# Kernel tuning notes

Measured on AMD Instinct MI355X. Metric: run time of the kernel, lower is better.

The kernel has to match this reference:

```python
import jax, jax.numpy as jnp
import numpy as np

N = 50000      # n_nodes
E = 800000     # n_edges (avg degree 16)
IN, HID, CLS = 128, 128, 40


def setup_inputs() -> dict:
    key = jax.random.key(0)
    ks = jax.random.split(key, 9)
    features = jax.random.normal(ks[0], (N, IN), dtype=jnp.float32)
    src = jax.random.randint(ks[1], (E,), 0, N)
    dst = jax.random.randint(ks[2], (E,), 0, N)
    # GraphConv weights (glorot-ish scale) and biases
    W0 = jax.random.normal(ks[3], (IN, HID), dtype=jnp.float32) / np.sqrt(IN).astype(np.float32)
    b0 = jnp.zeros((HID,), jnp.float32)
    W1 = jax.random.normal(ks[4], (HID, HID), dtype=jnp.float32) / np.sqrt(HID).astype(np.float32)
    b1 = jnp.zeros((HID,), jnp.float32)
    W2 = jax.random.normal(ks[5], (HID, CLS), dtype=jnp.float32) / np.sqrt(HID).astype(np.float32)
    b2 = jnp.zeros((CLS,), jnp.float32)
    return {"features": features, "src": src, "dst": dst,
            "W0": W0, "b0": b0, "W1": W1, "b1": b1, "W2": W2, "b2": b2}


def _degree_norms(src, dst, dtype):
    # DGL GraphConv norm='both': D_out^{-1/2} on source side, D_in^{-1/2} on dest side,
    # degrees clamped to a minimum of 1.
    ones = jnp.ones(src.shape[0], dtype)
    deg_out = jax.ops.segment_sum(ones, src, num_segments=N)
    deg_in = jax.ops.segment_sum(ones, dst, num_segments=N)
    norm_out = jnp.where(deg_out > 0, deg_out, 1.0) ** -0.5
    norm_in = jnp.where(deg_in > 0, deg_in, 1.0) ** -0.5
    return norm_out, norm_in


def _graph_conv(h, src, dst, norm_out, norm_in, W, b, act):
    # h' = D_in^{-1/2} A D_out^{-1/2} h W + b ; optional relu
    h = (h * norm_out[:, None]) @ W            # dense transform first (in >= out)
    agg = jax.ops.segment_sum(h[src], dst, num_segments=N)  # sparse aggregation
    out = agg * norm_in[:, None] + b
    return jax.nn.relu(out) if act else out


def reference(features, src, dst, W0, b0, W1, b1, W2, b2):
    norm_out, norm_in = _degree_norms(src, dst, features.dtype)
    # dropout is identity in eval mode
    h = _graph_conv(features, src, dst, norm_out, norm_in, W0, b0, True)
    h = _graph_conv(h, src, dst, norm_out, norm_in, W1, b1, True)
    h = _graph_conv(h, src, dst, norm_out, norm_in, W2, b2, False)
    return h
```

## Files before the change

kernel.cpp:

```cpp
#include <hip/hip_runtime.h>
#include <hip/hip_fp16.h>


static constexpr int NN  = 50000;
static constexpr int NE  = 800000;
static constexpr int HID = 128;
static constexpr int CLS = 40;
static constexpr int CAP = 48;

static constexpr int NGEMM  = (NN + 127) / 128;
static constexpr int NBUILD = (NE + 255) / 256;
static constexpr int NPREP  = 8;

typedef __attribute__((ext_vector_type(8))) _Float16 f16x8;
typedef __attribute__((ext_vector_type(4))) float    f32x4;

__device__ __forceinline__ void gemm128_body(const float* __restrict__ X,
                                             const float* __restrict__ W,
                                             __half* __restrict__ Y,
                                             int tileIdx, float* As, float* Bs) {
    constexpr int BSTR = 132;
    const int tid = threadIdx.x;
    const int rowBase = tileIdx * 128;

    const int bkk = tid >> 3;
    const int bc4 = tid & 7;
    const float* wrow = W + (size_t)bkk * 128 + bc4 * 16;

    const int rt = tid & 15;
    const int ct = tid >> 4;

    float acc[8][8];
    #pragma unroll
    for (int j = 0; j < 8; ++j)
        #pragma unroll
        for (int i = 0; i < 8; ++i) acc[j][i] = 0.f;

    float4 xv[4], wv[4];

    auto loadA = [&](int s) {
        #pragma unroll
        for (int i = 0; i < 4; ++i) {
            int f = tid + 256 * i;
            int r = f >> 3;
            int kc = f & 7;
            int grow = rowBase + r;
            xv[i] = (grow < NN)
                ? *(const float4*)(X + (size_t)grow * 128 + s * 32 + kc * 4)
                : make_float4(0.f, 0.f, 0.f, 0.f);
        }
    };
    auto loadB = [&](int s) {
        const float* p = wrow + (size_t)s * 32 * 128;
        #pragma unroll
        for (int i = 0; i < 4; ++i) wv[i] = ((const float4*)p)[i];
    };
    auto writeLDS = [&]() {
        #pragma unroll
        for (int i = 0; i < 4; ++i) {
            int f = tid + 256 * i;
            int r = f >> 3;
            int kc = f & 7;
            int pc = ((r >> 2) + kc) & 31;
            int base = pc * 4 + (r & 3);
            const float* v = (const float*)&xv[i];
            #pragma unroll
            for (int c = 0; c < 4; ++c)
                As[(kc * 4 + c) * 128 + base] = v[c];
        }
        #pragma unroll
        for (int i = 0; i < 4; ++i)
            *(float4*)&Bs[bkk * BSTR + bc4 * 16 + i * 4] = wv[i];
    };

    loadA(0); loadB(0);
    for (int s = 0; s < 4; ++s) {
        writeLDS();
        __syncthreads();
        if (s < 3) { loadA(s + 1); loadB(s + 1); }
        #pragma unroll 8
        for (int k = 0; k < 32; ++k) {
            int kc = k >> 2;
            int pa0 = (rt + kc) & 31;
            int pa1 = (rt + 16 + kc) & 31;
            float4 a0 = *(const float4*)&As[k * 128 + pa0 * 4];
            float4 a1 = *(const float4*)&As[k * 128 + pa1 * 4];
            float4 b0 = *(const float4*)&Bs[k * BSTR + ct * 8];
            float4 b1 = *(const float4*)&Bs[k * BSTR + ct * 8 + 4];
            float a[8] = {a0.x, a0.y, a0.z, a0.w, a1.x, a1.y, a1.z, a1.w};
            float b[8] = {b0.x, b0.y, b0.z, b0.w, b1.x, b1.y, b1.z, b1.w};
            #pragma unroll
            for (int j = 0; j < 8; ++j)
                #pragma unroll
                for (int ii = 0; ii < 8; ++ii)
                    acc[j][ii] = fmaf(a[j], b[ii], acc[j][ii]);
        }
        __syncthreads();
    }
    union Pack { __half2 h2[4]; uint4 u; };
    #pragma unroll
    for (int j = 0; j < 8; ++j) {
        int row = rowBase + ((j < 4) ? (4 * rt + j) : (64 + 4 * rt + (j - 4)));
        if (row < NN) {
            Pack p;
            #pragma unroll
            for (int q = 0; q < 4; ++q)
                p.h2[q] = __halves2half2(__float2half_rn(acc[j][2 * q]),
                                         __float2half_rn(acc[j][2 * q + 1]));
            *(uint4*)(Y + (size_t)row * 128 + ct * 8) = p.u;
        }
    }
}

__global__ __launch_bounds__(256) void fused_kernel(const float* __restrict__ X,
                                                    const float* __restrict__ W0,
                                                    __half* __restrict__ Y,
                                                    const int* __restrict__ src,
                                                    const int* __restrict__ dst,
                                                    int* __restrict__ deg_out,
                                                    int* __restrict__ cnt,
                                                    unsigned short* __restrict__ colbkt,
                                                    const float* __restrict__ W1,
                                                    __half* __restrict__ W1t) {
    __shared__ float As[32 * 128];
    __shared__ float Bs[32 * 132];
    int b = blockIdx.x;
    if (b < NGEMM) {
        gemm128_body(X, W0, Y, b, As, Bs);
    } else if (b < NGEMM + NBUILD) {
        int e = (b - NGEMM) * 256 + threadIdx.x;
        if (e < NE) {
            int s = src[e], d = dst[e];
            atomicAdd(&deg_out[s], 1);
            int slot = atomicAdd(&cnt[d], 1);
            if (slot < CAP) colbkt[(size_t)d * CAP + slot] = (unsigned short)s;
        }
    } else {
        int gid = (b - NGEMM - NBUILD) * 256 + threadIdx.x;
        int n = gid >> 4, q = gid & 15;
        union { __half h[8]; uint4 u; } p;
        #pragma unroll
        for (int j = 0; j < 8; ++j)
            p.h[j] = __float2half_rn(W1[(size_t)(q * 8 + j) * 128 + n]);
        ((uint4*)W1t)[n * 16 + ((q + n) & 15)] = p.u;
    }
}

__global__ __launch_bounds__(256) void gemm1_mfma(const __half* __restrict__ H,
                                                  const __half* __restrict__ W1t,
                                                  const float* __restrict__ norm_out,
                                                  __half* __restrict__ T) {
    __shared__ __half Ws[128 * 128];
    const int tid = threadIdx.x;
    #pragma unroll
    for (int i = 0; i < 8; ++i)
        ((uint4*)Ws)[tid + 256 * i] = ((const uint4*)W1t)[tid + 256 * i];

    const int wv   = tid >> 6;
    const int lane = tid & 63;
    const int m    = lane & 15;
    const int quad = lane >> 4;
    const int rowW = blockIdx.x * 64 + wv * 16;

    union AB { uint4 u; f16x8 h; };
    AB a[4];
    int arow = rowW + m;
    if (arow >= NN) arow = NN - 1;
    const uint4* hp = (const uint4*)(H + (size_t)arow * 128);
    #pragma unroll
    for (int kc = 0; kc < 4; ++kc)
        a[kc].u = hp[kc * 4 + quad];

    __syncthreads();

    f32x4 acc[8];
    #pragma unroll
    for (int nt = 0; nt < 8; ++nt) acc[nt] = (f32x4){0.f, 0.f, 0.f, 0.f};

    #pragma unroll
    for (int kc = 0; kc < 4; ++kc) {
        #pragma unroll
        for (int nt = 0; nt < 8; ++nt) {
            int n = nt * 16 + m;
            int q = kc * 4 + quad;
            AB bf;
            bf.u = ((const uint4*)Ws)[n * 16 + ((q + n) & 15)];
            acc[nt] = __builtin_amdgcn_mfma_f32_16x16x32_f16(a[kc].h, bf.h, acc[nt], 0, 0, 0);
        }
    }

    float nmv[4];
    #pragma unroll
    for (int r = 0; r < 4; ++r) {
        int row = rowW + quad * 4 + r;
        nmv[r] = (row < NN) ? norm_out[row] : 0.f;
    }
    #pragma unroll
    for (int nt = 0; nt < 8; ++nt) {
        int coln = nt * 16 + m;
        #pragma unroll
        for (int r = 0; r < 4; ++r) {
            int row = rowW + quad * 4 + r;
            if (row < NN)
                T[(size_t)row * 128 + coln] = __float2half_rn(acc[nt][r] * nmv[r]);
        }
    }
}

__global__ __launch_bounds__(256) void gemm40_kernel(const __half* __restrict__ X,
                                                     const float* __restrict__ W,
                                                     const float* __restrict__ norm_out,
                                                     __half* __restrict__ Y) {
    __shared__ float As[32 * 128];
    __shared__ float Bs[32 * 40];
    const int tid = threadIdx.x;
    const int rowBase = blockIdx.x * 128;

    const int rt = tid & 31;
    const int ct = tid >> 5;

    float acc[4][5];
    #pragma unroll
    for (int j = 0; j < 4; ++j)
        #pragma unroll
        for (int c = 0; c < 5; ++c) acc[j][c] = 0.f;

    uint4 xu[2];
    float4 wv[2];

    auto loadA = [&](int s) {
        #pragma unroll
        for (int i = 0; i < 2; ++i) {
            int f = tid + 256 * i;
            int r = f >> 2;
            int c = f & 3;
            int grow = rowBase + r;
            xu[i] = (grow < NN)
                ? *(const uint4*)(X + (size_t)grow * 128 + s * 32 + c * 8)
                : make_uint4(0, 0, 0, 0);
        }
    };
    auto loadB = [&](int s) {
        #pragma unroll
        for (int i = 0; i < 2; ++i) {
            int f = tid + 256 * i;
            if (f < 320) {
                int kk = f / 10, c4 = f - kk * 10;
                wv[i] = *(const float4*)(W + (size_t)(s * 32 + kk) * 40 + c4 * 4);
            }
        }
    };
    auto writeLDS = [&]() {
        #pragma unroll
        for (int i = 0; i < 2; ++i) {
            int f = tid + 256 * i;
            int r = f >> 2;
            int c = f & 3;
            const __half2* hp = (const __half2*)&xu[i];
            #pragma unroll
            for (int q = 0; q < 4; ++q) {
                float2 f2 = __half22float2(hp[q]);
                int k0 = c * 8 + 2 * q;
                int pc = ((r >> 2) + (k0 >> 2)) & 31;
                As[k0 * 128 + pc * 4 + (r & 3)]       = f2.x;
                As[(k0 + 1) * 128 + pc * 4 + (r & 3)] = f2.y;
            }
        }
        #pragma unroll
        for (int i = 0; i < 2; ++i) {
            int f = tid + 256 * i;
            if (f < 320) {
                int kk = f / 10, c4 = f - kk * 10;
                *(float4*)&Bs[kk * 40 + c4 * 4] = wv[i];
            }
        }
    };

    loadA(0); loadB(0);
    for (int s = 0; s < 4; ++s) {
        writeLDS();
        __syncthreads();
        if (s < 3) { loadA(s + 1); loadB(s + 1); }
        #pragma unroll 8
        for (int k = 0; k < 32; ++k) {
            int kc = k >> 2;
            int pa = (rt + kc) & 31;
            float4 av4 = *(const float4*)&As[k * 128 + pa * 4];
            float av[4] = {av4.x, av4.y, av4.z, av4.w};
            float bv[5];
            #pragma unroll
            for (int c = 0; c < 5; ++c) bv[c] = Bs[k * 40 + ct * 5 + c];
            #pragma unroll
            for (int j = 0; j < 4; ++j)
                #pragma unroll
                for (int c = 0; c < 5; ++c)
                    acc[j][c] = fmaf(av[j], bv[c], acc[j][c]);
        }
        __syncthreads();
    }
    #pragma unroll
    for (int j = 0; j < 4; ++j) {
        int row = rowBase + rt * 4 + j;
        if (row < NN) {
            float nm = norm_out[row];
            #pragma unroll
            for (int c = 0; c < 5; ++c)
                Y[(size_t)row * 40 + ct * 5 + c] = __float2half_rn(acc[j][c] * nm);
        }
    }
}

__global__ __launch_bounds__(256) void norm_scale_kernel(const int* __restrict__ deg_out,
                                                         const int* __restrict__ cnt,
                                                         float* __restrict__ norm_out,
                                                         float* __restrict__ norm_in,
                                                         __half* __restrict__ t) {
    __shared__ float nms[32];
    int base = blockIdx.x * 32;
    int tid = threadIdx.x;
    if (tid < 32) {
        int v = base + tid;
        float no = 1.f;
        if (v < NN) {
            int dof = deg_out[v], dif = cnt[v];
            no = rsqrtf((float)(dof > 0 ? dof : 1));
            norm_out[v] = no;
            norm_in[v]  = rsqrtf((float)(dif > 0 ? dif : 1));
        }
        nms[tid] = no;
    }
    __syncthreads();
    for (int i = tid; i < 512; i += 256) {
        int ro = i >> 4, ch = i & 15;
        int v = base + ro;
        if (v < NN) {
            uint4* p = (uint4*)t + (size_t)v * 16 + ch;
            uint4 u = *p;
            float nm = nms[ro];
            __half2* hp = (__half2*)&u;
            #pragma unroll
            for (int q = 0; q < 4; ++q) {
                float2 f = __half22float2(hp[q]);
                hp[q] = __halves2half2(__float2half_rn(f.x * nm),
                                       __float2half_rn(f.y * nm));
            }
            *p = u;
        }
    }
}

__global__ __launch_bounds__(256) void agg128h_kernel(const __half* __restrict__ T,
                                                      const unsigned short* __restrict__ colbkt,
                                                      const int* __restrict__ cnt,
                                                      const float* __restrict__ norm_in,
                                                      const float* __restrict__ bias,
                                                      __half* __restrict__ out) {
    int node = blockIdx.x * 4 + (threadIdx.x >> 6);
    int lane = threadIdx.x & 63;
    if (node >= NN) return;
    int dg = cnt[node];
    if (dg > CAP) dg = CAP;
    const unsigned short* bkt = colbkt + (size_t)node * CAP;
    const int grp = lane >> 4;
    const int l16 = lane & 15;

    float acc[8];
    #pragma unroll
    for (int i = 0; i < 8; ++i) acc[i] = 0.f;

    constexpr int B = 4;
    for (int j = 0; j < dg; j += 4 * B) {
        uint4 v[B];
        float w[B];
        #pragma unroll
        for (int u = 0; u < B; ++u) {
            int e  = j + 4 * u + grp;
            int ec = e < dg ? e : dg - 1;
            int s  = (int)bkt[ec];
            w[u]   = e < dg ? 1.f : 0.f;
            v[u]   = ((const uint4*)(T + (size_t)s * 128))[l16];
        }
        #pragma unroll
        for (int u = 0; u < B; ++u) {
            const __half2* hp = (const __half2*)&v[u];
            #pragma unroll
            for (int q = 0; q < 4; ++q) {
                float2 f = __half22float2(hp[q]);
                acc[2 * q]     = fmaf(f.x, w[u], acc[2 * q]);
                acc[2 * q + 1] = fmaf(f.y, w[u], acc[2 * q + 1]);
            }
        }
    }
    #pragma unroll
    for (int i = 0; i < 8; ++i) {
        acc[i] += __shfl_xor(acc[i], 16, 64);
        acc[i] += __shfl_xor(acc[i], 32, 64);
    }
    if (grp == 0) {
        float nm = norm_in[node];
        float4 b0 = ((const float4*)bias)[l16 * 2];
        float4 b1 = ((const float4*)bias)[l16 * 2 + 1];
        float o[8];
        o[0] = fmaf(acc[0], nm, b0.x); o[1] = fmaf(acc[1], nm, b0.y);
        o[2] = fmaf(acc[2], nm, b0.z); o[3] = fmaf(acc[3], nm, b0.w);
        o[4] = fmaf(acc[4], nm, b1.x); o[5] = fmaf(acc[5], nm, b1.y);
        o[6] = fmaf(acc[6], nm, b1.z); o[7] = fmaf(acc[7], nm, b1.w);
        union { __half2 h2[4]; uint4 u; } pk;
        #pragma unroll
        for (int q = 0; q < 4; ++q) {
            float x = fmaxf(o[2 * q], 0.f);
            float y = fmaxf(o[2 * q + 1], 0.f);
            pk.h2[q] = __halves2half2(__float2half_rn(x), __float2half_rn(y));
        }
        ((uint4*)(out + (size_t)node * 128))[l16] = pk.u;
    }
}

__global__ __launch_bounds__(256) void agg40h_kernel(const __half* __restrict__ T,
                                                     const unsigned short* __restrict__ colbkt,
                                                     const int* __restrict__ cnt,
                                                     const float* __restrict__ norm_in,
                                                     const float* __restrict__ bias,
                                                     float* __restrict__ out) {
    int node = blockIdx.x * 4 + (threadIdx.x >> 6);
    int lane = threadIdx.x & 63;
    if (node >= NN) return;
    int dg = cnt[node];
    if (dg > CAP) dg = CAP;
    const unsigned short* bkt = colbkt + (size_t)node * CAP;
    const int grp = lane / 20;
    const int l20 = lane - grp * 20;

    float accx = 0.f, accy = 0.f;
    constexpr int B = 4;
    for (int j = 0; j < dg; j += 3 * B) {
        unsigned int v[B];
        float w[B];
        #pragma unroll
        for (int u = 0; u < B; ++u) {
            int e  = j + 3 * u + grp;
            bool p = (grp < 3) && (e < dg);
            int ec = e < dg ? e : dg - 1;
            int s  = (grp < 3) ? (int)bkt[ec] : 0;
            w[u]   = p ? 1.f : 0.f;
            v[u]   = *(const unsigned int*)(T + (size_t)s * 40 + l20 * 2);
        }
        #pragma unroll
        for (int u = 0; u < B; ++u) {
            float2 f = __half22float2(*(const __half2*)&v[u]);
            accx = fmaf(f.x, w[u], accx);
            accy = fmaf(f.y, w[u], accy);
        }
    }
    accx += __shfl(accx, lane + 20, 64) + __shfl(accx, lane + 40, 64);
    accy += __shfl(accy, lane + 20, 64) + __shfl(accy, lane + 40, 64);

    if (lane < 20) {
        float nm = norm_in[node];
        float2 b = *(const float2*)(bias + lane * 2);
        float ox = fmaf(accx, nm, b.x);
        float oy = fmaf(accy, nm, b.y);
        *(float2*)(out + (size_t)node * 40 + lane * 2) = make_float2(ox, oy);
    }
}

extern "C" void kernel_launch(void* const* d_in, const int* in_sizes, int n_in,
                              void* d_out, int out_size, void* d_ws, size_t ws_size,
                              hipStream_t stream) {
    const float* features = (const float*)d_in[0];
    const int*   src      = (const int*)d_in[1];
    const int*   dst      = (const int*)d_in[2];
    const float* W0       = (const float*)d_in[3];
    const float* b0       = (const float*)d_in[4];
    const float* W1       = (const float*)d_in[5];
    const float* b1       = (const float*)d_in[6];
    const float* W2       = (const float*)d_in[7];
    const float* b2       = (const float*)d_in[8];
    float*       out      = (float*)d_out;

    char* ws = (char*)d_ws;
    auto alloc = [&](size_t bytes) {
        char* p = ws;
        ws += (bytes + 511) & ~(size_t)511;
        return p;
    };
    int*            deg_out  = (int*)alloc((size_t)NN * 4);
    int*            cnt      = (int*)alloc((size_t)NN * 4);
    float*          norm_out = (float*)alloc((size_t)NN * 4);
    float*          norm_in  = (float*)alloc((size_t)NN * 4);
    unsigned short* colbkt   = (unsigned short*)alloc((size_t)NN * CAP * 2);
    __half*         W1t      = (__half*)alloc((size_t)HID * HID * 2);
    __half*         t        = (__half*)alloc((size_t)NN * HID * 2);
    __half*         h        = (__half*)alloc((size_t)NN * HID * 2);
    if ((size_t)(ws - (char*)d_ws) > ws_size) return;

    hipMemsetAsync(deg_out, 0, (size_t)NN * 4, stream);
    hipMemsetAsync(cnt, 0, (size_t)NN * 4, stream);

    int gAgg = (NN + 3) / 4;

    fused_kernel<<<NGEMM + NBUILD + NPREP, 256, 0, stream>>>(
        features, W0, t, src, dst, deg_out, cnt, colbkt, W1, W1t);
    norm_scale_kernel<<<(NN + 31) / 32, 256, 0, stream>>>(deg_out, cnt, norm_out, norm_in, t);

    agg128h_kernel<<<gAgg, 256, 0, stream>>>(t, colbkt, cnt, norm_in, b0, h);
    gemm1_mfma<<<(NN + 63) / 64, 256, 0, stream>>>(h, W1t, norm_out, t);
    agg128h_kernel<<<gAgg, 256, 0, stream>>>(t, colbkt, cnt, norm_in, b1, h);
    gemm40_kernel<<<NGEMM, 256, 0, stream>>>(h, W2, norm_out, t);
    agg40h_kernel<<<gAgg, 256, 0, stream>>>(t, colbkt, cnt, norm_in, b2, out);
}
```

Before: 294.3 us.

## Fuse neighbor aggregation with following MFMA GEMM per 64-node block

Merges each 128-wide aggregation with the next layer's dense transform. Aggregated rows are kept in LDS and multiplied with MFMA f16 against pre-transposed W1 or W2, so the intermediate h buffer is never written to or re-read from global memory, and two launches are removed. W2 is converted to a padded, swizzled f16 layout inside the fused prep kernel, which replaces the scalar fp32 gemm40 kernel with MFMA. Each wave now aggregates 16 nodes two at a time instead of one node per wave. This lowers parallelism and may reduce latency hiding for the gather, and the 48 KB of shared memory per block limits occupancy.

After: 326.4 us. +10.9%, slower.

```diff
diff --git a/kernel.cpp b/kernel.cpp
--- a/kernel.cpp
+++ b/kernel.cpp
@@ -10,10 +10,13 @@
 
 static constexpr int NGEMM  = (NN + 127) / 128;
 static constexpr int NBUILD = (NE + 255) / 256;
-static constexpr int NPREP  = 8;
+static constexpr int NPREP1 = 8;
+static constexpr int NPREP2 = 3;
+static constexpr int NBLK64 = (NN + 63) / 64;
 
 typedef __attribute__((ext_vector_type(8))) _Float16 f16x8;
 typedef __attribute__((ext_vector_type(4))) float    f32x4;
+union ABu { uint4 u; f16x8 h; };
 
 __device__ __forceinline__ void gemm128_body(const float* __restrict__ X,
                                              const float* __restrict__ W,
@@ -121,7 +124,9 @@
                                                     int* __restrict__ cnt,
                                                     unsigned short* __restrict__ colbkt,
                                                     const float* __restrict__ W1,
-                                                    __half* __restrict__ W1t) {
+                                                    __half* __restrict__ W1t,
+                                                    const float* __restrict__ W2,
+                                                    __half* __restrict__ W2t) {
     __shared__ float As[32 * 128];
     __shared__ float Bs[32 * 132];
     int b = blockIdx.x;
@@ -135,7 +140,7 @@
             int slot = atomicAdd(&cnt[d], 1);
             if (slot < CAP) colbkt[(size_t)d * CAP + slot] = (unsigned short)s;
         }
-    } else {
+    } else if (b < NGEMM + NBUILD + NPREP1) {
         int gid = (b - NGEMM - NBUILD) * 256 + threadIdx.x;
         int n = gid >> 4, q = gid & 15;
         union { __half h[8]; uint4 u; } p;
@@ -143,170 +148,15 @@
         for (int j = 0; j < 8; ++j)
             p.h[j] = __float2half_rn(W1[(size_t)(q * 8 + j) * 128 + n]);
         ((uint4*)W1t)[n * 16 + ((q + n) & 15)] = p.u;
-    }
-}
-
-__global__ __launch_bounds__(256) void gemm1_mfma(const __half* __restrict__ H,
-                                                  const __half* __restrict__ W1t,
-                                                  const float* __restrict__ norm_out,
-                                                  __half* __restrict__ T) {
-    __shared__ __half Ws[128 * 128];
-    const int tid = threadIdx.x;
-    #pragma unroll
-    for (int i = 0; i < 8; ++i)
-        ((uint4*)Ws)[tid + 256 * i] = ((const uint4*)W1t)[tid + 256 * i];
-
-    const int wv   = tid >> 6;
-    const int lane = tid & 63;
-    const int m    = lane & 15;
-    const int quad = lane >> 4;
-    const int rowW = blockIdx.x * 64 + wv * 16;
-
-    union AB { uint4 u; f16x8 h; };
-    AB a[4];
-    int arow = rowW + m;
-    if (arow >= NN) arow = NN - 1;
-    const uint4* hp = (const uint4*)(H + (size_t)arow * 128);
-    #pragma unroll
-    for (int kc = 0; kc < 4; ++kc)
-        a[kc].u = hp[kc * 4 + quad];
-
-    __syncthreads();
-
-    f32x4 acc[8];
-    #pragma unroll
-    for (int nt = 0; nt < 8; ++nt) acc[nt] = (f32x4){0.f, 0.f, 0.f, 0.f};
-
-    #pragma unroll
-    for (int kc = 0; kc < 4; ++kc) {
-        #pragma unroll
-        for (int nt = 0; nt < 8; ++nt) {
-            int n = nt * 16 + m;
-            int q = kc * 4 + quad;
-            AB bf;
-            bf.u = ((const uint4*)Ws)[n * 16 + ((q + n) & 15)];
-            acc[nt] = __builtin_amdgcn_mfma_f32_16x16x32_f16(a[kc].h, bf.h, acc[nt], 0, 0, 0);
-        }
-    }
-
-    float nmv[4];
-    #pragma unroll
-    for (int r = 0; r < 4; ++r) {
-        int row = rowW + quad * 4 + r;
-        nmv[r] = (row < NN) ? norm_out[row] : 0.f;
-    }
-    #pragma unroll
-    for (int nt = 0; nt < 8; ++nt) {
-        int coln = nt * 16 + m;
-        #pragma unroll
-        for (int r = 0; r < 4; ++r) {
-            int row = rowW + quad * 4 + r;
-            if (row < NN)
-                T[(size_t)row * 128 + coln] = __float2half_rn(acc[nt][r] * nmv[r]);
-        }
-    }
-}
-
-__global__ __launch_bounds__(256) void gemm40_kernel(const __half* __restrict__ X,
-                                                     const float* __restrict__ W,
-                                                     const float* __restrict__ norm_out,
-                                                     __half* __restrict__ Y) {
-    __shared__ float As[32 * 128];
-    __shared__ float Bs[32 * 40];
-    const int tid = threadIdx.x;
-    const int rowBase = blockIdx.x * 128;
-
-    const int rt = tid & 31;
-    const int ct = tid >> 5;
-
-    float acc[4][5];
-    #pragma unroll
-    for (int j = 0; j < 4; ++j)
-        #pragma unroll
-        for (int c = 0; c < 5; ++c) acc[j][c] = 0.f;
-
-    uint4 xu[2];
-    float4 wv[2];
-
-    auto loadA = [&](int s) {
-        #pragma unroll
-        for (int i = 0; i < 2; ++i) {
-            int f = tid + 256 * i;
-            int r = f >> 2;
-            int c = f & 3;
-            int grow = rowBase + r;
-            xu[i] = (grow < NN)
-                ? *(const uint4*)(X + (size_t)grow * 128 + s * 32 + c * 8)
-                : make_uint4(0, 0, 0, 0);
-        }
-    };
-    auto loadB = [&](int s) {
-        #pragma unroll
-        for (int i = 0; i < 2; ++i) {
-            int f = tid + 256 * i;
-            if (f < 320) {
-                int kk = f / 10, c4 = f - kk * 10;
-                wv[i] = *(const float4*)(W + (size_t)(s * 32 + kk) * 40 + c4 * 4);
-            }
-        }
-    };
-    auto writeLDS = [&]() {
-        #pragma unroll
-        for (int i = 0; i < 2; ++i) {
-            int f = tid + 256 * i;
-            int r = f >> 2;
-            int c = f & 3;
-            const __half2* hp = (const __half2*)&xu[i];
-            #pragma unroll
-            for (int q = 0; q < 4; ++q) {
-                float2 f2 = __half22float2(hp[q]);
-                int k0 = c * 8 + 2 * q;
-                int pc = ((r >> 2) + (k0 >> 2)) & 31;
-                As[k0 * 128 + pc * 4 + (r & 3)]       = f2.x;
-                As[(k0 + 1) * 128 + pc * 4 + (r & 3)] = f2.y;
-            }
-        }
-        #pragma unroll
-        for (int i = 0; i < 2; ++i) {
-            int f = tid + 256 * i;
-            if (f < 320) {
-                int kk = f / 10, c4 = f - kk * 10;
-                *(float4*)&Bs[kk * 40 + c4 * 4] = wv[i];
-            }
-        }
-    };
-
-    loadA(0); loadB(0);
-    for (int s = 0; s < 4; ++s) {
-        writeLDS();
-        __syncthreads();
-        if (s < 3) { loadA(s + 1); loadB(s + 1); }
-        #pragma unroll 8
-        for (int k = 0; k < 32; ++k) {
-            int kc = k >> 2;
-            int pa = (rt + kc) & 31;
-            float4 av4 = *(const float4*)&As[k * 128 + pa * 4];
-            float av[4] = {av4.x, av4.y, av4.z, av4.w};
-            float bv[5];
-            #pragma unroll
-            for (int c = 0; c < 5; ++c) bv[c] = Bs[k * 40 + ct * 5 + c];
-            #pragma unroll
-            for (int j = 0; j < 4; ++j)
-                #pragma unroll
-                for (int c = 0; c < 5; ++c)
-                    acc[j][c] = fmaf(av[j], bv[c], acc[j][c]);
-        }
-        __syncthreads();
-    }
-    #pragma unroll
-    for (int j = 0; j < 4; ++j) {
-        int row = rowBase + rt * 4 + j;
-        if (row < NN) {
-            float nm = norm_out[row];
-            #pragma unroll
-            for (int c = 0; c < 5; ++c)
-                Y[(size_t)row * 40 + ct * 5 + c] = __float2half_rn(acc[j][c] * nm);
-        }
+    } else {
+        int gid = (b - NGEMM - NBUILD - NPREP1) * 256 + threadIdx.x;
+        int n = gid >> 4, q = gid & 15;
+        union { __half h[8]; uint4 u; } p;
+        #pragma unroll
+        for (int j = 0; j < 8; ++j)
+            p.h[j] = (n < CLS) ? __float2half_rn(W2[(size_t)(q * 8 + j) * CLS + n])
+                               : __half(0.f);
+        ((uint4*)W2t)[n * 16 + ((q + n) & 15)] = p.u;
     }
 }
 
@@ -349,71 +199,174 @@
     }
 }
 
-__global__ __launch_bounds__(256) void agg128h_kernel(const __half* __restrict__ T,
-                                                      const unsigned short* __restrict__ colbkt,
-                                                      const int* __restrict__ cnt,
-                                                      const float* __restrict__ norm_in,
-                                                      const float* __restrict__ bias,
-                                                      __half* __restrict__ out) {
-    int node = blockIdx.x * 4 + (threadIdx.x >> 6);
-    int lane = threadIdx.x & 63;
-    if (node >= NN) return;
-    int dg = cnt[node];
-    if (dg > CAP) dg = CAP;
-    const unsigned short* bkt = colbkt + (size_t)node * CAP;
-    const int grp = lane >> 4;
-    const int l16 = lane & 15;
-
-    float acc[8];
-    #pragma unroll
-    for (int i = 0; i < 8; ++i) acc[i] = 0.f;
-
-    constexpr int B = 4;
-    for (int j = 0; j < dg; j += 4 * B) {
-        uint4 v[B];
-        float w[B];
-        #pragma unroll
-        for (int u = 0; u < B; ++u) {
-            int e  = j + 4 * u + grp;
-            int ec = e < dg ? e : dg - 1;
-            int s  = (int)bkt[ec];
-            w[u]   = e < dg ? 1.f : 0.f;
-            v[u]   = ((const uint4*)(T + (size_t)s * 128))[l16];
-        }
-        #pragma unroll
-        for (int u = 0; u < B; ++u) {
-            const __half2* hp = (const __half2*)&v[u];
-            #pragma unroll
-            for (int q = 0; q < 4; ++q) {
-                float2 f = __half22float2(hp[q]);
-                acc[2 * q]     = fmaf(f.x, w[u], acc[2 * q]);
-                acc[2 * q + 1] = fmaf(f.y, w[u], acc[2 * q + 1]);
+template <int NT, int OST>
+__device__ __forceinline__ void agg_gemm_body(const __half* __restrict__ T,
+                                              const unsigned short* __restrict__ colbkt,
+                                              const int* __restrict__ cnt,
+                                              const float* __restrict__ norm_in,
+                                              const float* __restrict__ bias,
+                                              const float* __restrict__ norm_out,
+                                              __half* __restrict__ Y,
+                                              const __half* Ws, __half* Hs) {
+    const int tid  = threadIdx.x;
+    const int wv   = tid >> 6, lane = tid & 63;
+    const int grp  = lane >> 4, l16 = lane & 15;
+    const int rbase = wv * 16;
+    const int nodeBase = blockIdx.x * 64 + rbase;
+
+    const float4 bb0 = ((const float4*)bias)[l16 * 2];
+    const float4 bb1 = ((const float4*)bias)[l16 * 2 + 1];
+
+    for (int i0 = 0; i0 < 16; i0 += 2) {
+        int nodeA = nodeBase + i0;
+        int nodeB = nodeA + 1;
+        int dgA = 0, dgB = 0;
+        if (nodeA < NN) { dgA = cnt[nodeA]; if (dgA > CAP) dgA = CAP; }
+        if (nodeB < NN) { dgB = cnt[nodeB]; if (dgB > CAP) dgB = CAP; }
+        const unsigned short* bktA = colbkt + (size_t)(nodeA < NN ? nodeA : 0) * CAP;
+        const unsigned short* bktB = colbkt + (size_t)(nodeB < NN ? nodeB : 0) * CAP;
+        float accA[8], accB[8];
+        #pragma unroll
+        for (int q = 0; q < 8; ++q) { accA[q] = 0.f; accB[q] = 0.f; }
+        int dgM = dgA > dgB ? dgA : dgB;
+        for (int j = 0; j < dgM; j += 16) {
+            uint4 vA[4], vB[4];
+            float wA[4], wB[4];
+            #pragma unroll
+            for (int u = 0; u < 4; ++u) {
+                int e  = j + 4 * u + grp;
+                int eA = e < dgA ? e : 0;  wA[u] = e < dgA ? 1.f : 0.f;
+                int eB = e < dgB ? e : 0;  wB[u] = e < dgB ? 1.f : 0.f;
+                int sA = (int)bktA[eA];
+                int sB = (int)bktB[eB];
+                vA[u] = ((const uint4*)(T + (size_t)sA * 128))[l16];
+                vB[u] = ((const uint4*)(T + (size_t)sB * 128))[l16];
             }
-        }
-    }
-    #pragma unroll
-    for (int i = 0; i < 8; ++i) {
-        acc[i] += __shfl_xor(acc[i], 16, 64);
-        acc[i] += __shfl_xor(acc[i], 32, 64);
-    }
-    if (grp == 0) {
-        float nm = norm_in[node];
-        float4 b0 = ((const float4*)bias)[l16 * 2];
-        float4 b1 = ((const float4*)bias)[l16 * 2 + 1];
-        float o[8];
-        o[0] = fmaf(acc[0], nm, b0.x); o[1] = fmaf(acc[1], nm, b0.y);
-        o[2] = fmaf(acc[2], nm, b0.z); o[3] = fmaf(acc[3], nm, b0.w);
-        o[4] = fmaf(acc[4], nm, b1.x); o[5] = fmaf(acc[5], nm, b1.y);
-        o[6] = fmaf(acc[6], nm, b1.z); o[7] = fmaf(acc[7], nm, b1.w);
-        union { __half2 h2[4]; uint4 u; } pk;
-        #pragma unroll
-        for (int q = 0; q < 4; ++q) {
-            float x = fmaxf(o[2 * q], 0.f);
-            float y = fmaxf(o[2 * q + 1], 0.f);
-            pk.h2[q] = __halves2half2(__float2half_rn(x), __float2half_rn(y));
-        }
-        ((uint4*)(out + (size_t)node * 128))[l16] = pk.u;
-    }
+            #pragma unroll
+            for (int u = 0; u < 4; ++u) {
+                const __half2* ha = (const __half2*)&vA[u];
+                const __half2* hb = (const __half2*)&vB[u];
+                #pragma unroll
+                for (int q = 0; q < 4; ++q) {
+                    float2 fa = __half22float2(ha[q]);
+                    float2 fb = __half22float2(hb[q]);
+                    accA[2 * q]     = fmaf(fa.x, wA[u], accA[2 * q]);
+                    accA[2 * q + 1] = fmaf(fa.y, wA[u], accA[2 * q + 1]);
+                    accB[2 * q]     = fmaf(fb.x, wB[u], accB[2 * q]);
+                    accB[2 * q + 1] = fmaf(fb.y, wB[u], accB[2 * q + 1]);
+                }
+            }
+        }
+        #pragma unroll
+        for (int q = 0; q < 8; ++q) {
+            accA[q] += __shfl_xor(accA[q], 16, 64);
+            accA[q] += __shfl_xor(accA[q], 32, 64);
+            accB[q] += __shfl_xor(accB[q], 16, 64);
+            accB[q] += __shfl_xor(accB[q], 32, 64);
+        }
+        if (grp == 0) {
+            #pragma unroll
+            for (int p = 0; p < 2; ++p) {
+                int node = (p == 0) ? nodeA : nodeB;
+                const float* ac = (p == 0) ? accA : accB;
+                int r = rbase + i0 + p;
+                union { __half2 h2[4]; uint4 u; } pk;
+                if (node < NN) {
+                    float nm = norm_in[node];
+                    float o[8];
+                    o[0] = fmaf(ac[0], nm, bb0.x); o[1] = fmaf(ac[1], nm, bb0.y);
+                    o[2] = fmaf(ac[2], nm, bb0.z); o[3] = fmaf(ac[3], nm, bb0.w);
+                    o[4] = fmaf(ac[4], nm, bb1.x); o[5] = fmaf(ac[5], nm, bb1.y);
+                    o[6] = fmaf(ac[6], nm, bb1.z); o[7] = fmaf(ac[7], nm, bb1.w);
+                    #pragma unroll
+                    for (int q = 0; q < 4; ++q)
+                        pk.h2[q] = __halves2half2(
+                            __float2half_rn(fmaxf(o[2 * q],     0.f)),
+                            __float2half_rn(fmaxf(o[2 * q + 1], 0.f)));
+                } else {
+                    pk.u = make_uint4(0, 0, 0, 0);
+                }
+                ((uint4*)Hs)[r * 16 + ((l16 + r) & 15)] = pk.u;
+            }
+        }
+    }
+    __syncthreads();
+
+    const int m = l16, quad = grp;
+    ABu a[4];
+    #pragma unroll
+    for (int kc = 0; kc < 4; ++kc) {
+        int r = rbase + m;
+        int c = kc * 4 + quad;
+        a[kc].u = ((const uint4*)Hs)[r * 16 + ((c + r) & 15)];
+    }
+    f32x4 acc[NT];
+    #pragma unroll
+    for (int nt = 0; nt < NT; ++nt) acc[nt] = (f32x4){0.f, 0.f, 0.f, 0.f};
+    #pragma unroll
+    for (int kc = 0; kc < 4; ++kc) {
+        #pragma unroll
+        for (int nt = 0; nt < NT; ++nt) {
+            int n = nt * 16 + m;
+            int q = kc * 4 + quad;
+            ABu bf;
+            bf.u = ((const uint4*)Ws)[n * 16 + ((q + n) & 15)];
+            acc[nt] = __builtin_amdgcn_mfma_f32_16x16x32_f16(a[kc].h, bf.h, acc[nt], 0, 0, 0);
+        }
+    }
+    const int rowW = nodeBase;
+    float nmv[4];
+    #pragma unroll
+    for (int r = 0; r < 4; ++r) {
+        int row = rowW + quad * 4 + r;
+        nmv[r] = (row < NN) ? norm_out[row] : 0.f;
+    }
+    #pragma unroll
+    for (int nt = 0; nt < NT; ++nt) {
+        int coln = nt * 16 + m;
+        if (coln < OST) {
+            #pragma unroll
+            for (int r = 0; r < 4; ++r) {
+                int row = rowW + quad * 4 + r;
+                if (row < NN)
+                    Y[(size_t)row * OST + coln] = __float2half_rn(acc[nt][r] * nmv[r]);
+            }
+        }
+    }
+}
+
+__global__ __launch_bounds__(256) void agg_gemm1_kernel(const __half* __restrict__ T,
+                                                        const unsigned short* __restrict__ colbkt,
+                                                        const int* __restrict__ cnt,
+                                                        const float* __restrict__ norm_in,
+                                                        const float* __restrict__ bias,
+                                                        const __half* __restrict__ W1t,
+                                                        const float* __restrict__ norm_out,
+                                                        __half* __restrict__ Y) {
+    __shared__ __half Ws[128 * 128];
+    __shared__ __half Hs[64 * 128];
+    const int tid = threadIdx.x;
+    #pragma unroll
+    for (int i = 0; i < 8; ++i)
+        ((uint4*)Ws)[tid + 256 * i] = ((const uint4*)W1t)[tid + 256 * i];
+    agg_gemm_body<8, 128>(T, colbkt, cnt, norm_in, bias, norm_out, Y, Ws, Hs);
+}
+
+__global__ __launch_bounds__(256) void agg_gemm40_kernel(const __half* __restrict__ T,
+                                                         const unsigned short* __restrict__ colbkt,
+                                                         const int* __restrict__ cnt,
+                                                         const float* __restrict__ norm_in,
+                                                         const float* __restrict__ bias,
+                                                         const __half* __restrict__ W2t,
+                                                         const float* __restrict__ norm_out,
+                                                         __half* __restrict__ Y) {
+    __shared__ __half Ws[48 * 128];
+    __shared__ __half Hs[64 * 128];
+    const int tid = threadIdx.x;
+    #pragma unroll
+    for (int i = 0; i < 3; ++i)
+        ((uint4*)Ws)[tid + 256 * i] = ((const uint4*)W2t)[tid + 256 * i];
+    agg_gemm_body<3, 40>(T, colbkt, cnt, norm_in, bias, norm_out, Y, Ws, Hs);
 }
 
 __global__ __launch_bounds__(256) void agg40h_kernel(const __half* __restrict__ T,
@@ -490,22 +443,20 @@
     float*          norm_in  = (float*)alloc((size_t)NN * 4);
     unsigned short* colbkt   = (unsigned short*)alloc((size_t)NN * CAP * 2);
     __half*         W1t      = (__half*)alloc((size_t)HID * HID * 2);
+    __half*         W2t      = (__half*)alloc((size_t)48 * HID * 2);
     __half*         t        = (__half*)alloc((size_t)NN * HID * 2);
-    __half*         h        = (__half*)alloc((size_t)NN * HID * 2);
+    __half*         t2       = (__half*)alloc((size_t)NN * HID * 2);
+    __half*         t40      = (__half*)alloc((size_t)NN * CLS * 2);
     if ((size_t)(ws - (char*)d_ws) > ws_size) return;
 
     hipMemsetAsync(deg_out, 0, (size_t)NN * 4, stream);
     hipMemsetAsync(cnt, 0, (size_t)NN * 4, stream);
 
-    int gAgg = (NN + 3) / 4;
-
-    fused_kernel<<<NGEMM + NBUILD + NPREP, 256, 0, stream>>>(
-        features, W0, t, src, dst, deg_out, cnt, colbkt, W1, W1t);
+    fused_kernel<<<NGEMM + NBUILD + NPREP1 + NPREP2, 256, 0, stream>>>(
+        features, W0, t, src, dst, deg_out, cnt, colbkt, W1, W1t, W2, W2t);
     norm_scale_kernel<<<(NN + 31) / 32, 256, 0, stream>>>(deg_out, cnt, norm_out, norm_in, t);
 
-    agg128h_kernel<<<gAgg, 256, 0, stream>>>(t, colbkt, cnt, norm_in, b0, h);
-    gemm1_mfma<<<(NN + 63) / 64, 256, 0, stream>>>(h, W1t, norm_out, t);
-    agg128h_kernel<<<gAgg, 256, 0, stream>>>(t, colbkt, cnt, norm_in, b1, h);
-    gemm40_kernel<<<NGEMM, 256, 0, stream>>>(h, W2, norm_out, t);
-    agg40h_kernel<<<gAgg, 256, 0, stream>>>(t, colbkt, cnt, norm_in, b2, out);
-}
+    agg_gemm1_kernel<<<NBLK64, 256, 0, stream>>>(t, colbkt, cnt, norm_in, b0, W1t, norm_out, t2);
+    agg_gemm40_kernel<<<NBLK64, 256, 0, stream>>>(t2, colbkt, cnt, norm_in, b1, W2t, norm_out, t40);
+    agg40h_kernel<<<(NN + 3) / 4, 256, 0, stream>>>(t40, colbkt, cnt, norm_in, b2, out);
+}
```
